# Optimization experiments

Hardware: AMD Instinct MI355X
Metric: run time of the kernel (lower is better)

## Reference

```python
import jax, jax.numpy as jnp
import numpy as np
import math

N_HEADS = 8
N_LEVELS = 3
N_POINTS = 4
D_MODEL = 128
D_HEAD = D_MODEL // N_HEADS  # 16
SHAPES = [(128, 128), (64, 64), (32, 32)]  # (H, W) per level
N = 1
LQ = 6400  # 80x80 BEV queries


def _xavier(k, shape):
    lim = math.sqrt(6.0 / (shape[0] + shape[1]))
    return jax.random.uniform(k, shape, jnp.float32, -lim, lim)


def _grid_init_bias():
    # faithful to _reset_parameters: per-head directional bias, scaled per point
    thetas = np.arange(N_HEADS, dtype=np.float32) * (2.0 * np.pi / N_HEADS)
    grid = np.stack([np.cos(thetas), np.sin(thetas)], -1)
    grid = grid / np.abs(grid).max(-1, keepdims=True)
    grid = np.tile(grid.reshape(N_HEADS, 1, 1, 2), (1, N_LEVELS, N_POINTS, 1))
    grid = grid * (np.arange(N_POINTS, dtype=np.float32) + 1.0).reshape(1, 1, N_POINTS, 1)
    return jnp.asarray(grid.reshape(-1), jnp.float32)


def setup_inputs() -> dict:
    key = jax.random.key(0)
    ks = jax.random.split(key, 12)
    query = jax.random.normal(ks[0], (N, LQ, D_MODEL), jnp.float32)
    reference_points = jax.random.uniform(ks[1], (N, LQ, N_LEVELS, 2), jnp.float32)
    feat0 = jax.random.normal(ks[2], (N, 128, SHAPES[0][0], SHAPES[0][1]), jnp.float32)
    feat1 = jax.random.normal(ks[3], (N, 128, SHAPES[1][0], SHAPES[1][1]), jnp.float32)
    feat2 = jax.random.normal(ks[4], (N, 64, SHAPES[2][0], SHAPES[2][1]), jnp.float32)
    input_spatial_shapes = jnp.array(SHAPES, jnp.int32)
    # torch inits weight to 0; use small random so grads wrt W_off are exercised
    W_off = jax.random.normal(ks[5], (N_HEADS * N_LEVELS * N_POINTS * 2, D_MODEL), jnp.float32) * 0.01
    b_off = _grid_init_bias()
    Wk0 = _xavier(ks[6], (128, 128)); bk0 = jnp.zeros((128,), jnp.float32)
    Wk1 = _xavier(ks[7], (128, 128)); bk1 = jnp.zeros((128,), jnp.float32)
    Wk2 = _xavier(ks[8], (128, 64)); bk2 = jnp.zeros((128,), jnp.float32)
    W_out = _xavier(ks[9], (128, 128)); b_out = jnp.zeros((128,), jnp.float32)
    return {
        'query': query, 'reference_points': reference_points,
        'feat0': feat0, 'feat1': feat1, 'feat2': feat2,
        'input_spatial_shapes': input_spatial_shapes,
        'W_off': W_off, 'b_off': b_off,
        'Wk0': Wk0, 'bk0': bk0, 'Wk1': Wk1, 'bk1': bk1, 'Wk2': Wk2, 'bk2': bk2,
        'W_out': W_out, 'b_out': b_out,
    }


def _bilinear_sample(feat, loc):
    # feat: (N, C, H, W); loc: (N, S, 2) in [0,1]; grid_sample align_corners=False, zero padding
    n, c, h, w = feat.shape
    x = loc[..., 0] * w - 0.5
    y = loc[..., 1] * h - 0.5
    x0 = jnp.floor(x); y0 = jnp.floor(y)
    wx = x - x0; wy = y - y0  # (N, S)
    x0i = x0.astype(jnp.int32); y0i = y0.astype(jnp.int32)
    flat = feat.reshape(n, c, h * w)

    def gather(xi, yi):
        valid = (xi >= 0) & (xi < w) & (yi >= 0) & (yi < h)
        idx = jnp.clip(yi, 0, h - 1) * w + jnp.clip(xi, 0, w - 1)
        v = jnp.take_along_axis(flat, idx[:, None, :], axis=2)  # (N, C, S)
        return v * valid[:, None, :].astype(feat.dtype)

    out = (gather(x0i, y0i) * ((1 - wx) * (1 - wy))[:, None, :]
           + gather(x0i + 1, y0i) * (wx * (1 - wy))[:, None, :]
           + gather(x0i, y0i + 1) * ((1 - wx) * wy)[:, None, :]
           + gather(x0i + 1, y0i + 1) * (wx * wy)[:, None, :])
    return out  # (N, C, S)


def _forward(query, reference_points, feat0, feat1, feat2, input_spatial_shapes,
             W_off, b_off, Wk0, bk0, Wk1, bk1, Wk2, bk2, W_out, b_out):
    n, lq, _ = query.shape
    off = (query @ W_off.T + b_off).reshape(n, lq, N_HEADS, N_LEVELS, N_POINTS, 2)
    shp = input_spatial_shapes.astype(query.dtype)
    norm = jnp.stack([shp[:, 1], shp[:, 0]], -1)  # (L, 2) = (W, H)
    # sampling locations in [0,1]: (N, Lq, H, L, P, 2)
    loc = reference_points[:, :, None, :, None, :] + off / norm[None, None, None, :, None, :]
    qh = query.reshape(n, lq, N_HEADS, D_HEAD)
    feats = [feat0, feat1, feat2]
    Wks = [Wk0, Wk1, Wk2]
    bks = [bk0, bk1, bk2]
    logits, vals = [], []
    for l in range(N_LEVELS):
        c = feats[l].shape[1]
        ll = loc[:, :, :, l, :, :].reshape(n, lq * N_HEADS * N_POINTS, 2)
        s = _bilinear_sample(feats[l], ll)  # (N, C, Lq*H*P)
        s = s.reshape(n, c, lq, N_HEADS, N_POINTS).transpose(0, 2, 3, 4, 1)  # (N, Lq, H, P, C)
        # per-head key projection: head h uses its 16-dim slice of the 128-d projection
        k = jnp.einsum('nqhpc,hdc->nqhpd', s, Wks[l].reshape(N_HEADS, D_HEAD, c))
        k = k + bks[l].reshape(N_HEADS, D_HEAD)[None, None, :, None, :]
        logits.append(jnp.einsum('nqhd,nqhpd->nqhp', qh, k))
        vals.append(k)
    logits = jnp.stack(logits, 3)  # (N, Lq, H, L, P)
    vals = jnp.stack(vals, 3)      # (N, Lq, H, L, P, D_HEAD)
    scale = 1.0 / math.sqrt(D_HEAD)
    attn = jax.nn.softmax((logits * scale).reshape(n, lq, N_HEADS, N_LEVELS * N_POINTS), -1)
    attn = attn.reshape(n, lq, N_HEADS, N_LEVELS, N_POINTS)
    out = jnp.einsum('nqhlp,nqhlpd->nqhd', attn, vals).reshape(n, lq, D_MODEL)
    out = out @ W_out.T + b_out
    return out.transpose(1, 0, 2)  # (Lq, N, C) per output.permute(1,0,2)


def reference(query, reference_points, feat0, feat1, feat2, input_spatial_shapes,
              W_off, b_off, Wk0, bk0, Wk1, bk1, Wk2, bk2, W_out, b_out):
    return _forward(query, reference_points, feat0, feat1, feat2, input_spatial_shapes,
                    W_off, b_off, Wk0, bk0, Wk1, bk1, Wk2, bk2, W_out, b_out)
```

## Files before the change

kernel.cpp:

```cpp
#include <hip/hip_runtime.h>
#include <hip/hip_bf16.h>
#include <math.h>

#define LQ 6400

template<int C>
__global__ __launch_bounds__(256) void proj2_kernel(
    const float* __restrict__ fA, const float* __restrict__ fB,
    const float* __restrict__ WA, const float* __restrict__ WB,
    __hip_bfloat16* __restrict__ PA, __hip_bfloat16* __restrict__ PB,
    int splitB, int HWA, int HWB)
{
    constexpr int CI4 = C / 4;
    __shared__ float wk_sh[64 * C];
    __shared__ float f_sh[C * 64];
    int b = blockIdx.x;
    const float* feat; const float* Wk; __hip_bfloat16* P; int HW, local;
    if (b < splitB) { feat = fA; Wk = WA; P = PA; HW = HWA; local = b; }
    else            { feat = fB; Wk = WB; P = PB; HW = HWB; local = b - splitB; }
    int pblk = local >> 1;
    int half = local & 1;
    int cbase = half * 64;
    int p0 = pblk * 64;
    int tid = threadIdx.x;

    for (int idx = tid; idx < 64 * CI4; idx += 256) {
        int rl = idx / CI4;
        int ci4 = idx % CI4;
        float4 v = *reinterpret_cast<const float4*>(&Wk[(cbase + rl) * C + ci4 * 4]);
        *reinterpret_cast<float4*>(&wk_sh[rl * C + ((ci4 ^ (rl & (CI4 - 1))) << 2)]) = v;
    }
    for (int idx = tid; idx < C * 16; idx += 256) {
        int ci = idx >> 4;
        int pp4 = idx & 15;
        float4 v = *reinterpret_cast<const float4*>(&feat[ci * HW + p0 + pp4 * 4]);
        *reinterpret_cast<float4*>(&f_sh[ci * 64 + pp4 * 4]) = v;
    }
    __syncthreads();

    int c0 = tid & 31;
    int pg = tid >> 5;
    const int sw = c0 & (CI4 - 1);
    float acc[2][8];
    #pragma unroll
    for (int k = 0; k < 2; ++k)
        #pragma unroll
        for (int j = 0; j < 8; ++j) acc[k][j] = 0.f;

    #pragma unroll 4
    for (int ci4 = 0; ci4 < CI4; ++ci4) {
        float4 A0 = *reinterpret_cast<const float4*>(&wk_sh[c0 * C + ((ci4 ^ sw) << 2)]);
        float4 A1 = *reinterpret_cast<const float4*>(&wk_sh[(c0 + 32) * C + ((ci4 ^ sw) << 2)]);
        float a0v[4] = {A0.x, A0.y, A0.z, A0.w};
        float a1v[4] = {A1.x, A1.y, A1.z, A1.w};
        #pragma unroll
        for (int jj = 0; jj < 4; ++jj) {
            int ci = ci4 * 4 + jj;
            float4 Blo = *reinterpret_cast<const float4*>(&f_sh[ci * 64 + pg * 8]);
            float4 Bhi = *reinterpret_cast<const float4*>(&f_sh[ci * 64 + pg * 8 + 4]);
            float bv[8] = {Blo.x, Blo.y, Blo.z, Blo.w, Bhi.x, Bhi.y, Bhi.z, Bhi.w};
            #pragma unroll
            for (int j = 0; j < 8; ++j) {
                acc[0][j] = fmaf(a0v[jj], bv[j], acc[0][j]);
                acc[1][j] = fmaf(a1v[jj], bv[j], acc[1][j]);
            }
        }
    }
    #pragma unroll
    for (int k = 0; k < 2; ++k) {
        int co = cbase + c0 + 32 * k;
        #pragma unroll
        for (int j = 0; j < 8; ++j)
            P[(size_t)(p0 + pg * 8 + j) * 128 + co] = __float2bfloat16(acc[k][j]);
    }
}

__global__ __launch_bounds__(256) void off2_kernel(
    const float* __restrict__ query, const float* __restrict__ W_off,
    const float* __restrict__ b_off, float* __restrict__ offv)
{
    __shared__ float w_sh[96 * 128];
    __shared__ float q_sh[32 * 128];
    int b = blockIdx.x;
    int qblk = b >> 1;
    int half = b & 1;
    int rbase = half * 96;
    int q0 = qblk * 32;
    int tid = threadIdx.x;

    for (int idx = tid; idx < 96 * 32; idx += 256) {
        int rl = idx >> 5;
        int ci4 = idx & 31;
        float4 v = *reinterpret_cast<const float4*>(&W_off[(rbase + rl) * 128 + ci4 * 4]);
        *reinterpret_cast<float4*>(&w_sh[rl * 128 + ((ci4 ^ (rl & 31)) << 2)]) = v;
    }
    for (int idx = tid; idx < 32 * 32; idx += 256) {
        int qq = idx >> 5;
        int ci4 = idx & 31;
        *reinterpret_cast<float4*>(&q_sh[qq * 128 + ci4 * 4]) =
            *reinterpret_cast<const float4*>(&query[(q0 + qq) * 128 + ci4 * 4]);
    }
    __syncthreads();

    int c0 = tid & 31;
    int qg = tid >> 5;
    float acc[3][4];
    #pragma unroll
    for (int k = 0; k < 3; ++k)
        #pragma unroll
        for (int j = 0; j < 4; ++j) acc[k][j] = 0.f;

    #pragma unroll 4
    for (int ci4 = 0; ci4 < 32; ++ci4) {
        float4 A[3];
        #pragma unroll
        for (int k = 0; k < 3; ++k)
            A[k] = *reinterpret_cast<const float4*>(&w_sh[(c0 + 32 * k) * 128 + ((ci4 ^ c0) << 2)]);
        #pragma unroll
        for (int j = 0; j < 4; ++j) {
            float4 B = *reinterpret_cast<const float4*>(&q_sh[(qg * 4 + j) * 128 + ci4 * 4]);
            #pragma unroll
            for (int k = 0; k < 3; ++k) {
                acc[k][j] = fmaf(A[k].x, B.x, acc[k][j]);
                acc[k][j] = fmaf(A[k].y, B.y, acc[k][j]);
                acc[k][j] = fmaf(A[k].z, B.z, acc[k][j]);
                acc[k][j] = fmaf(A[k].w, B.w, acc[k][j]);
            }
        }
    }
    #pragma unroll
    for (int k = 0; k < 3; ++k) {
        int r = rbase + c0 + 32 * k;
        float bias = b_off[r];
        #pragma unroll
        for (int j = 0; j < 4; ++j)
            offv[(q0 + qg * 4 + j) * 192 + r] = acc[k][j] + bias;
    }
}

__global__ __launch_bounds__(256) void attn2_kernel(
    const float* __restrict__ query, const float* __restrict__ ref,
    const float* __restrict__ offv,
    const __hip_bfloat16* __restrict__ P0, const __hip_bfloat16* __restrict__ P1,
    const __hip_bfloat16* __restrict__ P2,
    const float* __restrict__ bk0, const float* __restrict__ bk1,
    const float* __restrict__ bk2,
    float* __restrict__ hout)
{
    __shared__ float q_sh[128];
    __shared__ float off_sh[192];
    __shared__ float ref_sh[6];
    __shared__ float bias_sh[3][128];
    __shared__ float logit_sh[8][12];
    __shared__ float k_sh[8][12][17];
    int q = blockIdx.x;
    int tid = threadIdx.x;
    if (tid < 128) {
        q_sh[tid] = query[q * 128 + tid];
        bias_sh[0][tid] = bk0[tid];
        bias_sh[1][tid] = bk1[tid];
        bias_sh[2][tid] = bk2[tid];
    }
    if (tid < 192) off_sh[tid] = offv[q * 192 + tid];
    if (tid < 6) ref_sh[tid] = ref[q * 6 + tid];
    __syncthreads();

    int grp = tid >> 4;
    int d = tid & 15;
    #pragma unroll
    for (int it = 0; it < 6; ++it) {
        int s = it * 16 + grp;
        int h = s / 12;
        int lp = s - h * 12;
        int l = lp >> 2;
        const __hip_bfloat16* P; int W, H;
        if (l == 0)      { P = P0; W = 128; H = 128; }
        else if (l == 1) { P = P1; W = 64;  H = 64;  }
        else             { P = P2; W = 32;  H = 32;  }
        float ox = off_sh[2 * s];
        float oy = off_sh[2 * s + 1];
        float rx = ref_sh[2 * l];
        float ry = ref_sh[2 * l + 1];
        float x = fmaf(rx, (float)W, ox) - 0.5f;
        float y = fmaf(ry, (float)H, oy) - 0.5f;
        float x0f = floorf(x), y0f = floorf(y);
        float wx = x - x0f, wy = y - y0f;
        int x0 = (int)x0f, y0 = (int)y0f;
        int x1 = x0 + 1, y1 = y0 + 1;
        float mx0 = (x0 >= 0 && x0 < W) ? 1.f : 0.f;
        float mx1 = (x1 >= 0 && x1 < W) ? 1.f : 0.f;
        float my0 = (y0 >= 0 && y0 < H) ? 1.f : 0.f;
        float my1 = (y1 >= 0 && y1 < H) ? 1.f : 0.f;
        int xc0 = min(max(x0, 0), W - 1), xc1 = min(max(x1, 0), W - 1);
        int yc0 = min(max(y0, 0), H - 1), yc1 = min(max(y1, 0), H - 1);
        int co = h * 16 + d;
        const __hip_bfloat16* base = P + co;
        float v00 = __bfloat162float(base[(size_t)(yc0 * W + xc0) * 128]);
        float v10 = __bfloat162float(base[(size_t)(yc0 * W + xc1) * 128]);
        float v01 = __bfloat162float(base[(size_t)(yc1 * W + xc0) * 128]);
        float v11 = __bfloat162float(base[(size_t)(yc1 * W + xc1) * 128]);
        float w00 = (1.f - wx) * (1.f - wy) * mx0 * my0;
        float w10 = wx * (1.f - wy) * mx1 * my0;
        float w01 = (1.f - wx) * wy * mx0 * my1;
        float w11 = wx * wy * mx1 * my1;
        float kv = fmaf(w00, v00, fmaf(w10, v10, fmaf(w01, v01, w11 * v11))) + bias_sh[l][co];
        float prod = q_sh[co] * kv;
        prod += __shfl_xor(prod, 1);
        prod += __shfl_xor(prod, 2);
        prod += __shfl_xor(prod, 4);
        prod += __shfl_xor(prod, 8);
        k_sh[h][lp][d] = kv;
        if (d == 0) logit_sh[h][lp] = prod;
    }
    __syncthreads();

    if (tid < 128) {
        int h = tid >> 4, dd = tid & 15;
        float m = -1e30f;
        #pragma unroll
        for (int j = 0; j < 12; ++j) m = fmaxf(m, logit_sh[h][j]);
        float ssum = 0.f, o = 0.f;
        #pragma unroll
        for (int j = 0; j < 12; ++j) {
            float e = __expf(0.25f * (logit_sh[h][j] - m));
            ssum += e;
            o = fmaf(e, k_sh[h][j][dd], o);
        }
        hout[q * 128 + tid] = o / ssum;
    }
}

__global__ __launch_bounds__(256) void outp2_kernel(
    const float* __restrict__ hin, const float* __restrict__ W_out,
    const float* __restrict__ b_out, float* __restrict__ out)
{
    __shared__ float w_sh[64 * 128];
    __shared__ float q_sh[64 * 128];
    int b = blockIdx.x;
    int qblk = b >> 1;
    int half = b & 1;
    int rbase = half * 64;
    int q0 = qblk * 64;
    int tid = threadIdx.x;

    for (int idx = tid; idx < 64 * 32; idx += 256) {
        int rl = idx >> 5;
        int ci4 = idx & 31;
        float4 v = *reinterpret_cast<const float4*>(&W_out[(rbase + rl) * 128 + ci4 * 4]);
        *reinterpret_cast<float4*>(&w_sh[rl * 128 + ((ci4 ^ (rl & 31)) << 2)]) = v;
    }
    for (int idx = tid; idx < 64 * 32; idx += 256) {
        int qq = idx >> 5;
        int ci4 = idx & 31;
        *reinterpret_cast<float4*>(&q_sh[qq * 128 + ci4 * 4]) =
            *reinterpret_cast<const float4*>(&hin[(q0 + qq) * 128 + ci4 * 4]);
    }
    __syncthreads();

    int c0 = tid & 31;
    int qg = tid >> 5;
    float acc[2][8];
    #pragma unroll
    for (int k = 0; k < 2; ++k)
        #pragma unroll
        for (int j = 0; j < 8; ++j) acc[k][j] = 0.f;

    #pragma unroll 4
    for (int ci4 = 0; ci4 < 32; ++ci4) {
        float4 A0 = *reinterpret_cast<const float4*>(&w_sh[c0 * 128 + ((ci4 ^ c0) << 2)]);
        float4 A1 = *reinterpret_cast<const float4*>(&w_sh[(c0 + 32) * 128 + ((ci4 ^ c0) << 2)]);
        #pragma unroll
        for (int j = 0; j < 8; ++j) {
            float4 B = *reinterpret_cast<const float4*>(&q_sh[(qg * 8 + j) * 128 + ci4 * 4]);
            acc[0][j] = fmaf(A0.x, B.x, acc[0][j]);
            acc[0][j] = fmaf(A0.y, B.y, acc[0][j]);
            acc[0][j] = fmaf(A0.z, B.z, acc[0][j]);
            acc[0][j] = fmaf(A0.w, B.w, acc[0][j]);
            acc[1][j] = fmaf(A1.x, B.x, acc[1][j]);
            acc[1][j] = fmaf(A1.y, B.y, acc[1][j]);
            acc[1][j] = fmaf(A1.z, B.z, acc[1][j]);
            acc[1][j] = fmaf(A1.w, B.w, acc[1][j]);
        }
    }
    #pragma unroll
    for (int k = 0; k < 2; ++k) {
        int r = rbase + c0 + 32 * k;
        float bias = b_out[r];
        #pragma unroll
        for (int j = 0; j < 8; ++j)
            out[(q0 + qg * 8 + j) * 128 + r] = acc[k][j] + bias;
    }
}

extern "C" void kernel_launch(void* const* d_in, const int* in_sizes, int n_in,
                              void* d_out, int out_size, void* d_ws, size_t ws_size,
                              hipStream_t stream) {
    const float* query = (const float*)d_in[0];
    const float* ref   = (const float*)d_in[1];
    const float* feat0 = (const float*)d_in[2];
    const float* feat1 = (const float*)d_in[3];
    const float* feat2 = (const float*)d_in[4];
    const float* W_off = (const float*)d_in[6];
    const float* b_off = (const float*)d_in[7];
    const float* Wk0   = (const float*)d_in[8];
    const float* bk0   = (const float*)d_in[9];
    const float* Wk1   = (const float*)d_in[10];
    const float* bk1   = (const float*)d_in[11];
    const float* Wk2   = (const float*)d_in[12];
    const float* bk2   = (const float*)d_in[13];
    const float* W_out = (const float*)d_in[14];
    const float* b_out = (const float*)d_in[15];
    float* out = (float*)d_out;

    __hip_bfloat16* P0 = (__hip_bfloat16*)d_ws;
    __hip_bfloat16* P1 = P0 + 16384 * 128;
    __hip_bfloat16* P2 = P1 + 4096 * 128;
    float* offv = (float*)(P2 + 1024 * 128);
    float* hout = offv + 6400 * 192;

    hipLaunchKernelGGL((proj2_kernel<128>), dim3(640), dim3(256), 0, stream,
                       feat0, feat1, Wk0, Wk1, P0, P1, 512, 16384, 4096);
    hipLaunchKernelGGL((proj2_kernel<64>), dim3(32), dim3(256), 0, stream,
                       feat2, feat2, Wk2, Wk2, P2, P2, 32, 1024, 1024);
    hipLaunchKernelGGL(off2_kernel, dim3(400), dim3(256), 0, stream,
                       query, W_off, b_off, offv);
    hipLaunchKernelGGL(attn2_kernel, dim3(6400), dim3(256), 0, stream,
                       query, ref, offv, P0, P1, P2, bk0, bk1, bk2, hout);
    hipLaunchKernelGGL(outp2_kernel, dim3(200), dim3(256), 0, stream,
                       hout, W_out, b_out, out);
}
```

Measured before the change: 161.4 us.

## Merge projection and offset kernels; restructure sampling with vectorized corner gathers

The three prep kernels (two key projections and the offset GEMM) are merged into one launch that dispatches on block index and shares one static shared-memory buffer. The attention kernel drops to 128 threads per query. Each group of 16 lanes now loads the four bilinear corners as 4-channel bf16 uint2 vectors, with all 12 gathers issued before any use, and combines them through shuffles. This aims to cut launch overhead and scattered scalar bf16 loads, in exchange for more registers and extra shuffle work.

```diff
diff --git a/kernel.cpp b/kernel.cpp
--- a/kernel.cpp
+++ b/kernel.cpp
@@ -4,20 +4,16 @@
 
 #define LQ 6400
 
+
 template<int C>
-__global__ __launch_bounds__(256) void proj2_kernel(
-    const float* __restrict__ fA, const float* __restrict__ fB,
-    const float* __restrict__ WA, const float* __restrict__ WB,
-    __hip_bfloat16* __restrict__ PA, __hip_bfloat16* __restrict__ PB,
-    int splitB, int HWA, int HWB)
+__device__ __forceinline__ void proj_body(
+    float* __restrict__ smem,
+    const float* __restrict__ feat, const float* __restrict__ Wk,
+    __hip_bfloat16* __restrict__ P, int HW, int local)
 {
     constexpr int CI4 = C / 4;
-    __shared__ float wk_sh[64 * C];
-    __shared__ float f_sh[C * 64];
-    int b = blockIdx.x;
-    const float* feat; const float* Wk; __hip_bfloat16* P; int HW, local;
-    if (b < splitB) { feat = fA; Wk = WA; P = PA; HW = HWA; local = b; }
-    else            { feat = fB; Wk = WB; P = PB; HW = HWB; local = b - splitB; }
+    float* wk_sh = smem;
+    float* f_sh  = smem + 64 * C;
     int pblk = local >> 1;
     int half = local & 1;
     int cbase = half * 64;
@@ -75,15 +71,15 @@
     }
 }
 
-__global__ __launch_bounds__(256) void off2_kernel(
+__device__ __forceinline__ void off_body(
+    float* __restrict__ smem,
     const float* __restrict__ query, const float* __restrict__ W_off,
-    const float* __restrict__ b_off, float* __restrict__ offv)
-{
-    __shared__ float w_sh[96 * 128];
-    __shared__ float q_sh[32 * 128];
-    int b = blockIdx.x;
-    int qblk = b >> 1;
-    int half = b & 1;
+    const float* __restrict__ b_off, float* __restrict__ offv, int local)
+{
+    float* w_sh = smem;
+    float* q_sh = smem + 96 * 128;
+    int qblk = local >> 1;
+    int half = local & 1;
     int rbase = half * 96;
     int q0 = qblk * 32;
     int tid = threadIdx.x;
@@ -138,7 +134,30 @@
     }
 }
 
-__global__ __launch_bounds__(256) void attn2_kernel(
+__global__ __launch_bounds__(256) void prep_kernel(
+    const float* __restrict__ feat0, const float* __restrict__ feat1,
+    const float* __restrict__ feat2,
+    const float* __restrict__ Wk0, const float* __restrict__ Wk1,
+    const float* __restrict__ Wk2,
+    __hip_bfloat16* __restrict__ P0, __hip_bfloat16* __restrict__ P1,
+    __hip_bfloat16* __restrict__ P2,
+    const float* __restrict__ query, const float* __restrict__ W_off,
+    const float* __restrict__ b_off, float* __restrict__ offv)
+{
+    __shared__ __align__(16) float smem[16384];
+    int b = blockIdx.x;
+    if (b < 512) {
+        proj_body<128>(smem, feat0, Wk0, P0, 16384, b);
+    } else if (b < 640) {
+        proj_body<128>(smem, feat1, Wk1, P1, 4096, b - 512);
+    } else if (b < 672) {
+        proj_body<64>(smem, feat2, Wk2, P2, 1024, b - 640);
+    } else {
+        off_body(smem, query, W_off, b_off, offv, b - 672);
+    }
+}
+
+__global__ __launch_bounds__(128) void attn3_kernel(
     const float* __restrict__ query, const float* __restrict__ ref,
     const float* __restrict__ offv,
     const __hip_bfloat16* __restrict__ P0, const __hip_bfloat16* __restrict__ P1,
@@ -151,91 +170,109 @@
     __shared__ float off_sh[192];
     __shared__ float ref_sh[6];
     __shared__ float bias_sh[3][128];
-    __shared__ float logit_sh[8][12];
-    __shared__ float k_sh[8][12][17];
+    __shared__ float logit_sh[96];
+    __shared__ __align__(16) float k_sh[8 * 196];
     int q = blockIdx.x;
     int tid = threadIdx.x;
-    if (tid < 128) {
-        q_sh[tid] = query[q * 128 + tid];
-        bias_sh[0][tid] = bk0[tid];
-        bias_sh[1][tid] = bk1[tid];
-        bias_sh[2][tid] = bk2[tid];
-    }
-    if (tid < 192) off_sh[tid] = offv[q * 192 + tid];
+    q_sh[tid] = query[q * 128 + tid];
+    bias_sh[0][tid] = bk0[tid];
+    bias_sh[1][tid] = bk1[tid];
+    bias_sh[2][tid] = bk2[tid];
+    off_sh[tid] = offv[q * 192 + tid];
+    if (tid < 64) off_sh[128 + tid] = offv[q * 192 + 128 + tid];
     if (tid < 6) ref_sh[tid] = ref[q * 6 + tid];
     __syncthreads();
 
-    int grp = tid >> 4;
-    int d = tid & 15;
-    #pragma unroll
-    for (int it = 0; it < 6; ++it) {
-        int s = it * 16 + grp;
-        int h = s / 12;
+    const int grp = tid >> 4;
+    const int d = tid & 15;
+    const int c = d >> 2;
+    const int quad = d & 3;
+    const int dxl = c & 1;
+    const int dyl = c >> 1;
+
+    uint2 raw[12];
+    float wcv[12];
+    #pragma unroll
+    for (int it = 0; it < 12; ++it) {
+        int s = it * 8 + grp;
+        int h = (s * 171) >> 11;
         int lp = s - h * 12;
         int l = lp >> 2;
-        const __hip_bfloat16* P; int W, H;
-        if (l == 0)      { P = P0; W = 128; H = 128; }
-        else if (l == 1) { P = P1; W = 64;  H = 64;  }
-        else             { P = P2; W = 32;  H = 32;  }
+        int W = 128 >> l;
         float ox = off_sh[2 * s];
         float oy = off_sh[2 * s + 1];
-        float rx = ref_sh[2 * l];
-        float ry = ref_sh[2 * l + 1];
-        float x = fmaf(rx, (float)W, ox) - 0.5f;
-        float y = fmaf(ry, (float)H, oy) - 0.5f;
+        float x = fmaf(ref_sh[2 * l], (float)W, ox) - 0.5f;
+        float y = fmaf(ref_sh[2 * l + 1], (float)W, oy) - 0.5f;
         float x0f = floorf(x), y0f = floorf(y);
         float wx = x - x0f, wy = y - y0f;
-        int x0 = (int)x0f, y0 = (int)y0f;
-        int x1 = x0 + 1, y1 = y0 + 1;
-        float mx0 = (x0 >= 0 && x0 < W) ? 1.f : 0.f;
-        float mx1 = (x1 >= 0 && x1 < W) ? 1.f : 0.f;
-        float my0 = (y0 >= 0 && y0 < H) ? 1.f : 0.f;
-        float my1 = (y1 >= 0 && y1 < H) ? 1.f : 0.f;
-        int xc0 = min(max(x0, 0), W - 1), xc1 = min(max(x1, 0), W - 1);
-        int yc0 = min(max(y0, 0), H - 1), yc1 = min(max(y1, 0), H - 1);
-        int co = h * 16 + d;
-        const __hip_bfloat16* base = P + co;
-        float v00 = __bfloat162float(base[(size_t)(yc0 * W + xc0) * 128]);
-        float v10 = __bfloat162float(base[(size_t)(yc0 * W + xc1) * 128]);
-        float v01 = __bfloat162float(base[(size_t)(yc1 * W + xc0) * 128]);
-        float v11 = __bfloat162float(base[(size_t)(yc1 * W + xc1) * 128]);
-        float w00 = (1.f - wx) * (1.f - wy) * mx0 * my0;
-        float w10 = wx * (1.f - wy) * mx1 * my0;
-        float w01 = (1.f - wx) * wy * mx0 * my1;
-        float w11 = wx * wy * mx1 * my1;
-        float kv = fmaf(w00, v00, fmaf(w10, v10, fmaf(w01, v01, w11 * v11))) + bias_sh[l][co];
-        float prod = q_sh[co] * kv;
-        prod += __shfl_xor(prod, 1);
-        prod += __shfl_xor(prod, 2);
-        prod += __shfl_xor(prod, 4);
-        prod += __shfl_xor(prod, 8);
-        k_sh[h][lp][d] = kv;
-        if (d == 0) logit_sh[h][lp] = prod;
-    }
-    __syncthreads();
-
-    if (tid < 128) {
-        int h = tid >> 4, dd = tid & 15;
-        float m = -1e30f;
-        #pragma unroll
-        for (int j = 0; j < 12; ++j) m = fmaxf(m, logit_sh[h][j]);
-        float ssum = 0.f, o = 0.f;
-        #pragma unroll
-        for (int j = 0; j < 12; ++j) {
-            float e = __expf(0.25f * (logit_sh[h][j] - m));
-            ssum += e;
-            o = fmaf(e, k_sh[h][j][dd], o);
+        int xs = (int)x0f + dxl;
+        int ys = (int)y0f + dyl;
+        float m = (xs >= 0 && xs < W && ys >= 0 && ys < W) ? 1.f : 0.f;
+        float fx = dxl ? wx : 1.f - wx;
+        float fy = dyl ? wy : 1.f - wy;
+        wcv[it] = fx * fy * m;
+        int xc = min(max(xs, 0), W - 1);
+        int yc = min(max(ys, 0), W - 1);
+        const __hip_bfloat16* P = (l == 0) ? P0 : ((l == 1) ? P1 : P2);
+        size_t idx = (size_t)(yc * W + xc) * 128 + h * 16 + quad * 4;
+        raw[it] = *reinterpret_cast<const uint2*>(P + idx);
+    }
+
+    #pragma unroll
+    for (int it = 0; it < 12; ++it) {
+        int s = it * 8 + grp;
+        int h = (s * 171) >> 11;
+        int lp = s - h * 12;
+        int l = lp >> 2;
+        unsigned a = raw[it].x, bb = raw[it].y;
+        float w = wcv[it];
+        float k0 = w * __uint_as_float(a << 16);
+        float k1 = w * __uint_as_float(a & 0xffff0000u);
+        float k2 = w * __uint_as_float(bb << 16);
+        float k3 = w * __uint_as_float(bb & 0xffff0000u);
+        k0 += __shfl_xor(k0, 4); k1 += __shfl_xor(k1, 4);
+        k2 += __shfl_xor(k2, 4); k3 += __shfl_xor(k3, 4);
+        k0 += __shfl_xor(k0, 8); k1 += __shfl_xor(k1, 8);
+        k2 += __shfl_xor(k2, 8); k3 += __shfl_xor(k3, 8);
+        int co4 = h * 16 + quad * 4;
+        k0 += bias_sh[l][co4 + 0];
+        k1 += bias_sh[l][co4 + 1];
+        k2 += bias_sh[l][co4 + 2];
+        k3 += bias_sh[l][co4 + 3];
+        float lg = q_sh[co4] * k0;
+        lg = fmaf(q_sh[co4 + 1], k1, lg);
+        lg = fmaf(q_sh[co4 + 2], k2, lg);
+        lg = fmaf(q_sh[co4 + 3], k3, lg);
+        lg += __shfl_xor(lg, 1);
+        lg += __shfl_xor(lg, 2);
+        if (d < 4) {
+            float4 kv = make_float4(k0, k1, k2, k3);
+            *reinterpret_cast<float4*>(&k_sh[h * 196 + lp * 16 + d * 4]) = kv;
         }
-        hout[q * 128 + tid] = o / ssum;
-    }
+        if (d == 0) logit_sh[h * 12 + lp] = lg;
+    }
+    __syncthreads();
+
+    int h2 = tid >> 4, dd = tid & 15;
+    float m = -1e30f;
+    #pragma unroll
+    for (int j = 0; j < 12; ++j) m = fmaxf(m, logit_sh[h2 * 12 + j]);
+    float ssum = 0.f, o = 0.f;
+    #pragma unroll
+    for (int j = 0; j < 12; ++j) {
+        float e = __expf(0.25f * (logit_sh[h2 * 12 + j] - m));
+        ssum += e;
+        o = fmaf(e, k_sh[h2 * 196 + j * 16 + dd], o);
+    }
+    hout[q * 128 + tid] = o / ssum;
 }
 
 __global__ __launch_bounds__(256) void outp2_kernel(
     const float* __restrict__ hin, const float* __restrict__ W_out,
     const float* __restrict__ b_out, float* __restrict__ out)
 {
-    __shared__ float w_sh[64 * 128];
-    __shared__ float q_sh[64 * 128];
+    __shared__ __align__(16) float w_sh[64 * 128];
+    __shared__ __align__(16) float q_sh[64 * 128];
     int b = blockIdx.x;
     int qblk = b >> 1;
     int half = b & 1;
@@ -318,13 +355,10 @@
     float* offv = (float*)(P2 + 1024 * 128);
     float* hout = offv + 6400 * 192;
 
-    hipLaunchKernelGGL((proj2_kernel<128>), dim3(640), dim3(256), 0, stream,
-                       feat0, feat1, Wk0, Wk1, P0, P1, 512, 16384, 4096);
-    hipLaunchKernelGGL((proj2_kernel<64>), dim3(32), dim3(256), 0, stream,
-                       feat2, feat2, Wk2, Wk2, P2, P2, 32, 1024, 1024);
-    hipLaunchKernelGGL(off2_kernel, dim3(400), dim3(256), 0, stream,
+    hipLaunchKernelGGL(prep_kernel, dim3(1072), dim3(256), 0, stream,
+                       feat0, feat1, feat2, Wk0, Wk1, Wk2, P0, P1, P2,
                        query, W_off, b_off, offv);
-    hipLaunchKernelGGL(attn2_kernel, dim3(6400), dim3(256), 0, stream,
+    hipLaunchKernelGGL(attn3_kernel, dim3(6400), dim3(128), 0, stream,
                        query, ref, offv, P0, P1, P2, bk0, bk1, bk2, hout);
     hipLaunchKernelGGL(outp2_kernel, dim3(200), dim3(256), 0, stream,
                        hout, W_out, b_out, out);
```

After: 157.9 us. 1.02x faster.
